# Performance work log

Measured on AMD Instinct MI355X. Metric: run time of the kernel, lower is better.

The kernel has to match this reference:

```python
import jax, jax.numpy as jnp
import numpy as np

H = 4        # num_heads
D = 16       # d_hid (per-head dim)
INF = 1e9


def setup_inputs() -> dict:
    key = jax.random.key(0)
    ks = jax.random.split(key, 8)
    T, R, DT, DZ = 4, 384, 64, 128
    t = jax.random.normal(ks[0], (T, R, R, DT), dtype=jnp.float32)
    z = jax.random.normal(ks[1], (R, R, DZ), dtype=jnp.float32)
    template_mask = jnp.ones((T,), dtype=jnp.float32)
    wq = jax.random.normal(ks[2], (DZ, H * D), dtype=jnp.float32) * 0.08
    wk = jax.random.normal(ks[3], (DT, H * D), dtype=jnp.float32) * 0.12
    wv = jax.random.normal(ks[4], (DT, H * D), dtype=jnp.float32) * 0.12
    wo = jax.random.normal(ks[5], (H * D, DZ), dtype=jnp.float32) * 0.12
    bo = jnp.zeros((DZ,), dtype=jnp.float32)
    return {"t": t, "z": z, "template_mask": template_mask,
            "wq": wq, "wk": wk, "wv": wv, "wo": wo, "bo": bo}


def reference(t, z, template_mask, wq, wk, wv, wo, bo):
    # t: [T, R, R, d_t], z: [R, R, d_z], template_mask: [T]
    R = z.shape[0]
    scale = 1.0 / np.sqrt(float(D))
    # gen_attn_mask: 0 where mask > 0, -inf where masked out
    bias = jnp.where(template_mask > 0.0, 0.0, -INF)          # [T]
    # permute_final_dims(t, (1,2,0,3)): template axis becomes kv length
    tp = jnp.transpose(t, (1, 2, 0, 3))                        # [R, R, T, d_t]
    # q_len is 1 (z.unsqueeze(-2)); fold it away
    q = (z @ wq).reshape(R, R, H, D) * scale                   # [R, R, H, D]
    k = (tp @ wk).reshape(R, R, -1, H, D)                      # [R, R, T, H, D]
    v = (tp @ wv).reshape(R, R, -1, H, D)                      # [R, R, T, H, D]
    logits = jnp.einsum('xyhd,xythd->xyht', q, k) + bias       # [R, R, H, T]
    a = jax.nn.softmax(logits, axis=-1)
    o = jnp.einsum('xyht,xythd->xyhd', a, v).reshape(R, R, H * D)
    return o @ wo + bo                                         # [R, R, d_z]
```

## Files before the change

### kernel.cpp

```cpp
#include <hip/hip_runtime.h>


typedef __bf16 bf16x8 __attribute__((ext_vector_type(8)));
typedef float f32x4 __attribute__((ext_vector_type(4)));
typedef unsigned int u32x4 __attribute__((ext_vector_type(4)));
typedef unsigned int u32x2 __attribute__((ext_vector_type(2)));

#define MFMA16(A, B, C) __builtin_amdgcn_mfma_f32_16x16x32_bf16((A), (B), (C), 0, 0, 0)

__device__ __forceinline__ unsigned int f2b_pk(float a, float b) {
  unsigned int ua = __float_as_uint(a), ub = __float_as_uint(b);
  ua = (ua + 0x7fffu + ((ua >> 16) & 1u)) >> 16;
  ub = (ub + 0x7fffu + ((ub >> 16) & 1u)) & 0xffff0000u;
  return ua | ub;
}

__device__ __forceinline__ bf16x8 ldg8(const float* p) {
  const float4* q = (const float4*)p;
  float4 a = q[0];
  float4 b = q[1];
  u32x4 u;
  u.x = f2b_pk(a.x, a.y);
  u.y = f2b_pk(a.z, a.w);
  u.z = f2b_pk(b.x, b.y);
  u.w = f2b_pk(b.z, b.w);
  return __builtin_bit_cast(bf16x8, u);
}

__device__ __forceinline__ bf16x8 ldsA(const char* smem, int baseByte, int row,
                                       int colElem, int strideElem) {
  int off = baseByte + (((row * strideElem + colElem) * 2) ^ ((row & 7) << 4));
  return __builtin_bit_cast(bf16x8, *(const u32x4*)(smem + off));
}

__global__ __launch_bounds__(256, 2)
void tpa_kernel(const float* __restrict__ t_, const float* __restrict__ z_,
                const float* __restrict__ mask_,
                const float* __restrict__ wq_, const float* __restrict__ wk_,
                const float* __restrict__ wv_, const float* __restrict__ wo_,
                const float* __restrict__ bo_, float* __restrict__ out_) {
  extern __shared__ char smem[];

  for (int i = threadIdx.x; i < 24576; i += 256) {
    float v;
    int off;
    if (i < 8192) {
      int r = i >> 7, cc = i & 127;
      v = wq_[cc * 64 + r] * 0.25f;
      off = 0 + ((i * 2) ^ ((r & 7) << 4));
    } else if (i < 12288) {
      int j = i - 8192, r = j >> 6, cc = j & 63;
      v = wk_[cc * 64 + r];
      off = 16384 + ((j * 2) ^ ((r & 7) << 4));
    } else if (i < 16384) {
      int j = i - 12288, r = j >> 6, cc = j & 63;
      v = wv_[cc * 64 + r];
      off = 24576 + ((j * 2) ^ ((r & 7) << 4));
    } else {
      int j = i - 16384, r = j >> 6, cc = j & 63;
      v = wo_[cc * 128 + r];
      off = 32768 + ((j * 2) ^ ((r & 7) << 4));
    }
    unsigned int u = __float_as_uint(v);
    *(unsigned short*)(smem + off) =
        (unsigned short)((u + 0x7fffu + ((u >> 16) & 1u)) >> 16);
  }
  __syncthreads();

  const int lane = threadIdx.x & 63;
  const int wid = threadIdx.x >> 6;
  const int c = lane & 15;
  const int g = lane >> 4;

  const float b0 = mask_[0] > 0.f ? 0.f : -1e9f;
  const float b1 = mask_[1] > 0.f ? 0.f : -1e9f;
  const float b2 = mask_[2] > 0.f ? 0.f : -1e9f;
  const float b3 = mask_[3] > 0.f ? 0.f : -1e9f;

  float4 bo_v[8];
#pragma unroll
  for (int m = 0; m < 8; ++m) bo_v[m] = *(const float4*)(bo_ + m * 16 + g * 4);

  char* Olds = smem + 49152 + wid * 2048;
  const f32x4 vz = {0.f, 0.f, 0.f, 0.f};

  for (int tile = blockIdx.x * 4 + wid; tile < 9216; tile += 2048) {
    const int p = tile * 16 + c;
    const float* zp = z_ + (size_t)p * 128;
    const float* tp = t_ + (size_t)p * 64;

    f32x4 qacc[4] = {vz, vz, vz, vz};
#pragma unroll
    for (int s = 0; s < 4; ++s) {
      bf16x8 zb = ldg8(zp + s * 32 + g * 8);
#pragma unroll
      for (int h = 0; h < 4; ++h)
        qacc[h] = MFMA16(ldsA(smem, 0, h * 16 + c, s * 32 + g * 8, 128), zb, qacc[h]);
    }

    f32x4 oacc[4] = {vz, vz, vz, vz};
    float ssum[4] = {0.f, 0.f, 0.f, 0.f};
#pragma unroll
    for (int tt = 0; tt < 4; ++tt) {
      const float* tq = tp + (size_t)tt * 9437184;
      bf16x8 tb0 = ldg8(tq + g * 8);
      bf16x8 tb1 = ldg8(tq + 32 + g * 8);
      f32x4 kacc[4] = {vz, vz, vz, vz};
      f32x4 vacc[4] = {vz, vz, vz, vz};
#pragma unroll
      for (int h = 0; h < 4; ++h) {
        kacc[h] = MFMA16(ldsA(smem, 16384, h * 16 + c, g * 8, 64), tb0, kacc[h]);
        kacc[h] = MFMA16(ldsA(smem, 16384, h * 16 + c, 32 + g * 8, 64), tb1, kacc[h]);
        vacc[h] = MFMA16(ldsA(smem, 24576, h * 16 + c, g * 8, 64), tb0, vacc[h]);
        vacc[h] = MFMA16(ldsA(smem, 24576, h * 16 + c, 32 + g * 8, 64), tb1, vacc[h]);
      }
      const float bt = (tt == 0) ? b0 : (tt == 1) ? b1 : (tt == 2) ? b2 : b3;
#pragma unroll
      for (int h = 0; h < 4; ++h) {
        float d = qacc[h][0] * kacc[h][0] + qacc[h][1] * kacc[h][1] +
                  qacc[h][2] * kacc[h][2] + qacc[h][3] * kacc[h][3];
        d += __shfl_xor(d, 16);
        d += __shfl_xor(d, 32);
        float e = __expf(d + bt);
        ssum[h] += e;
        oacc[h] += e * vacc[h];
      }
    }

#pragma unroll
    for (int h = 0; h < 4; ++h) {
      float inv = 1.0f / ssum[h];
      f32x4 o = oacc[h] * inv;
      u32x2 w;
      w.x = f2b_pk(o[0], o[1]);
      w.y = f2b_pk(o[2], o[3]);
      int off = (c * 128 + h * 32 + g * 8) ^ ((c & 7) << 4);
      *(u32x2*)(Olds + off) = w;
    }
    asm volatile("s_waitcnt lgkmcnt(0)" ::: "memory");

    f32x4 outacc[8] = {vz, vz, vz, vz, vz, vz, vz, vz};
#pragma unroll
    for (int s = 0; s < 2; ++s) {
      int off = (c * 128 + s * 64 + g * 16) ^ ((c & 7) << 4);
      bf16x8 ob = __builtin_bit_cast(bf16x8, *(const u32x4*)(Olds + off));
#pragma unroll
      for (int m = 0; m < 8; ++m)
        outacc[m] = MFMA16(ldsA(smem, 32768, m * 16 + c, s * 32 + g * 8, 64), ob, outacc[m]);
    }

    float* op = out_ + (size_t)p * 128;
#pragma unroll
    for (int m = 0; m < 8; ++m) {
      float4 bv = bo_v[m];
      float4 st;
      st.x = outacc[m][0] + bv.x;
      st.y = outacc[m][1] + bv.y;
      st.z = outacc[m][2] + bv.z;
      st.w = outacc[m][3] + bv.w;
      *(float4*)(op + m * 16 + g * 4) = st;
    }
    asm volatile("" ::: "memory");
  }
}

extern "C" void kernel_launch(void* const* d_in, const int* in_sizes, int n_in,
                              void* d_out, int out_size, void* d_ws, size_t ws_size,
                              hipStream_t stream) {
  const float* t = (const float*)d_in[0];
  const float* z = (const float*)d_in[1];
  const float* mk = (const float*)d_in[2];
  const float* wq = (const float*)d_in[3];
  const float* wk = (const float*)d_in[4];
  const float* wv = (const float*)d_in[5];
  const float* wo = (const float*)d_in[6];
  const float* bo = (const float*)d_in[7];
  float* out = (float*)d_out;
  (void)in_sizes; (void)n_in; (void)out_size; (void)d_ws; (void)ws_size;

  hipLaunchKernelGGL(tpa_kernel, dim3(512), dim3(256), 57344, stream,
                     t, z, mk, wq, wk, wv, wo, bo, out);
}
```

Baseline: 93.80 us.

## Double workgroup size, prefetch next template slice, and shrink register footprint

Raises the block to 512 threads (8 waves) with 64KB LDS and a launch bound of 4 blocks per SM, which doubles the waves resident per block. The t loads for the next template are software-prefetched while the current one is computed. K and V accumulators are now computed per head instead of all heads at once, and the bias is reloaded at store time rather than kept in registers. Together these aim to cut register pressure and raise memory-level parallelism, at the cost of more per-head MFMA dependency chains and larger LDS per block, which may limit blocks per CU.

```diff
diff --git a/kernel.cpp b/kernel.cpp
--- a/kernel.cpp
+++ b/kernel.cpp
@@ -15,10 +15,7 @@
   return ua | ub;
 }
 
-__device__ __forceinline__ bf16x8 ldg8(const float* p) {
-  const float4* q = (const float4*)p;
-  float4 a = q[0];
-  float4 b = q[1];
+__device__ __forceinline__ bf16x8 pack8(float4 a, float4 b) {
   u32x4 u;
   u.x = f2b_pk(a.x, a.y);
   u.y = f2b_pk(a.z, a.w);
@@ -27,13 +24,18 @@
   return __builtin_bit_cast(bf16x8, u);
 }
 
+__device__ __forceinline__ bf16x8 ldg8(const float* p) {
+  const float4* q = (const float4*)p;
+  return pack8(q[0], q[1]);
+}
+
 __device__ __forceinline__ bf16x8 ldsA(const char* smem, int baseByte, int row,
                                        int colElem, int strideElem) {
   int off = baseByte + (((row * strideElem + colElem) * 2) ^ ((row & 7) << 4));
   return __builtin_bit_cast(bf16x8, *(const u32x4*)(smem + off));
 }
 
-__global__ __launch_bounds__(256, 2)
+__global__ __launch_bounds__(512, 4)
 void tpa_kernel(const float* __restrict__ t_, const float* __restrict__ z_,
                 const float* __restrict__ mask_,
                 const float* __restrict__ wq_, const float* __restrict__ wk_,
@@ -41,7 +43,7 @@
                 const float* __restrict__ bo_, float* __restrict__ out_) {
   extern __shared__ char smem[];
 
-  for (int i = threadIdx.x; i < 24576; i += 256) {
+  for (int i = threadIdx.x; i < 24576; i += 512) {
     float v;
     int off;
     if (i < 8192) {
@@ -77,17 +79,18 @@
   const float b2 = mask_[2] > 0.f ? 0.f : -1e9f;
   const float b3 = mask_[3] > 0.f ? 0.f : -1e9f;
 
-  float4 bo_v[8];
-#pragma unroll
-  for (int m = 0; m < 8; ++m) bo_v[m] = *(const float4*)(bo_ + m * 16 + g * 4);
-
   char* Olds = smem + 49152 + wid * 2048;
   const f32x4 vz = {0.f, 0.f, 0.f, 0.f};
 
-  for (int tile = blockIdx.x * 4 + wid; tile < 9216; tile += 2048) {
+  for (int tile = blockIdx.x * 8 + wid; tile < 9216; tile += 4096) {
     const int p = tile * 16 + c;
     const float* zp = z_ + (size_t)p * 128;
     const float* tp = t_ + (size_t)p * 64;
+
+    float4 c0 = *(const float4*)(tp + g * 8);
+    float4 c1 = *(const float4*)(tp + g * 8 + 4);
+    float4 c2 = *(const float4*)(tp + 32 + g * 8);
+    float4 c3 = *(const float4*)(tp + 32 + g * 8 + 4);
 
     f32x4 qacc[4] = {vz, vz, vz, vz};
 #pragma unroll
@@ -102,29 +105,32 @@
     float ssum[4] = {0.f, 0.f, 0.f, 0.f};
 #pragma unroll
     for (int tt = 0; tt < 4; ++tt) {
-      const float* tq = tp + (size_t)tt * 9437184;
-      bf16x8 tb0 = ldg8(tq + g * 8);
-      bf16x8 tb1 = ldg8(tq + 32 + g * 8);
-      f32x4 kacc[4] = {vz, vz, vz, vz};
-      f32x4 vacc[4] = {vz, vz, vz, vz};
-#pragma unroll
-      for (int h = 0; h < 4; ++h) {
-        kacc[h] = MFMA16(ldsA(smem, 16384, h * 16 + c, g * 8, 64), tb0, kacc[h]);
-        kacc[h] = MFMA16(ldsA(smem, 16384, h * 16 + c, 32 + g * 8, 64), tb1, kacc[h]);
-        vacc[h] = MFMA16(ldsA(smem, 24576, h * 16 + c, g * 8, 64), tb0, vacc[h]);
-        vacc[h] = MFMA16(ldsA(smem, 24576, h * 16 + c, 32 + g * 8, 64), tb1, vacc[h]);
+      float4 n0, n1, n2, n3;
+      if (tt < 3) {
+        const float* tn = tp + (size_t)(tt + 1) * 9437184;
+        n0 = *(const float4*)(tn + g * 8);
+        n1 = *(const float4*)(tn + g * 8 + 4);
+        n2 = *(const float4*)(tn + 32 + g * 8);
+        n3 = *(const float4*)(tn + 32 + g * 8 + 4);
       }
+      bf16x8 tb0 = pack8(c0, c1);
+      bf16x8 tb1 = pack8(c2, c3);
       const float bt = (tt == 0) ? b0 : (tt == 1) ? b1 : (tt == 2) ? b2 : b3;
 #pragma unroll
       for (int h = 0; h < 4; ++h) {
-        float d = qacc[h][0] * kacc[h][0] + qacc[h][1] * kacc[h][1] +
-                  qacc[h][2] * kacc[h][2] + qacc[h][3] * kacc[h][3];
+        f32x4 kacc = MFMA16(ldsA(smem, 16384, h * 16 + c, g * 8, 64), tb0, vz);
+        kacc = MFMA16(ldsA(smem, 16384, h * 16 + c, 32 + g * 8, 64), tb1, kacc);
+        float d = qacc[h][0] * kacc[0] + qacc[h][1] * kacc[1] +
+                  qacc[h][2] * kacc[2] + qacc[h][3] * kacc[3];
         d += __shfl_xor(d, 16);
         d += __shfl_xor(d, 32);
         float e = __expf(d + bt);
         ssum[h] += e;
-        oacc[h] += e * vacc[h];
+        f32x4 vacc = MFMA16(ldsA(smem, 24576, h * 16 + c, g * 8, 64), tb0, vz);
+        vacc = MFMA16(ldsA(smem, 24576, h * 16 + c, 32 + g * 8, 64), tb1, vacc);
+        oacc[h] += e * vacc;
       }
+      if (tt < 3) { c0 = n0; c1 = n1; c2 = n2; c3 = n3; }
     }
 
 #pragma unroll
@@ -150,9 +156,10 @@
     }
 
     float* op = out_ + (size_t)p * 128;
+    const float4* bop = (const float4*)bo_;
 #pragma unroll
     for (int m = 0; m < 8; ++m) {
-      float4 bv = bo_v[m];
+      float4 bv = bop[m * 4 + g];
       float4 st;
       st.x = outacc[m][0] + bv.x;
       st.y = outacc[m][1] + bv.y;
@@ -178,6 +185,6 @@
   float* out = (float*)d_out;
   (void)in_sizes; (void)n_in; (void)out_size; (void)d_ws; (void)ws_size;
 
-  hipLaunchKernelGGL(tpa_kernel, dim3(512), dim3(256), 57344, stream,
+  hipLaunchKernelGGL(tpa_kernel, dim3(512), dim3(512), 65536, stream,
                      t, z, mk, wq, wk, wv, wo, bo, out);
 }
```

New measurement: 161.7 us. 72.4% more time.

## Split Q projection into separate kernel via workspace to raise occupancy

Applied to the files above, without the earlier changes.

Moves the z@wq projection into its own kernel that writes bf16 Q into the workspace. The main attention kernel then reads Q, needs less LDS and fewer registers, and runs with launch bounds of 4 blocks and 768 blocks instead of 2 and 512. The goal is higher occupancy and better latency hiding on the streaming t loads. The cost is an extra kernel launch plus a round trip of Q through global memory (about 19 MB written and read). The original fused kernel is kept as a fallback when the workspace is too small.

```diff
diff --git a/kernel.cpp b/kernel.cpp
--- a/kernel.cpp
+++ b/kernel.cpp
@@ -15,10 +15,7 @@
   return ua | ub;
 }
 
-__device__ __forceinline__ bf16x8 ldg8(const float* p) {
-  const float4* q = (const float4*)p;
-  float4 a = q[0];
-  float4 b = q[1];
+__device__ __forceinline__ bf16x8 pack8(float4 a, float4 b) {
   u32x4 u;
   u.x = f2b_pk(a.x, a.y);
   u.y = f2b_pk(a.z, a.w);
@@ -27,75 +24,102 @@
   return __builtin_bit_cast(bf16x8, u);
 }
 
+__device__ __forceinline__ bf16x8 ldg8(const float* p) {
+  const float4* q = (const float4*)p;
+  return pack8(q[0], q[1]);
+}
+
 __device__ __forceinline__ bf16x8 ldsA(const char* smem, int baseByte, int row,
                                        int colElem, int strideElem) {
   int off = baseByte + (((row * strideElem + colElem) * 2) ^ ((row & 7) << 4));
   return __builtin_bit_cast(bf16x8, *(const u32x4*)(smem + off));
 }
 
-__global__ __launch_bounds__(256, 2)
-void tpa_kernel(const float* __restrict__ t_, const float* __restrict__ z_,
-                const float* __restrict__ mask_,
-                const float* __restrict__ wq_, const float* __restrict__ wk_,
-                const float* __restrict__ wv_, const float* __restrict__ wo_,
-                const float* __restrict__ bo_, float* __restrict__ out_) {
+__device__ __forceinline__ void stage_w(char* smem, int off, float v, int r, int j) {
+  unsigned int u = __float_as_uint(v);
+  *(unsigned short*)(smem + off + ((j * 2) ^ ((r & 7) << 4))) =
+      (unsigned short)((u + 0x7fffu + ((u >> 16) & 1u)) >> 16);
+}
+
+__global__ __launch_bounds__(256, 4)
+void q_kernel(const float* __restrict__ z_, const float* __restrict__ wq_,
+              u32x2* __restrict__ q_) {
   extern __shared__ char smem[];
-
-  for (int i = threadIdx.x; i < 24576; i += 256) {
-    float v;
-    int off;
-    if (i < 8192) {
-      int r = i >> 7, cc = i & 127;
-      v = wq_[cc * 64 + r] * 0.25f;
-      off = 0 + ((i * 2) ^ ((r & 7) << 4));
-    } else if (i < 12288) {
-      int j = i - 8192, r = j >> 6, cc = j & 63;
-      v = wk_[cc * 64 + r];
-      off = 16384 + ((j * 2) ^ ((r & 7) << 4));
-    } else if (i < 16384) {
-      int j = i - 12288, r = j >> 6, cc = j & 63;
-      v = wv_[cc * 64 + r];
-      off = 24576 + ((j * 2) ^ ((r & 7) << 4));
-    } else {
-      int j = i - 16384, r = j >> 6, cc = j & 63;
-      v = wo_[cc * 128 + r];
-      off = 32768 + ((j * 2) ^ ((r & 7) << 4));
-    }
-    unsigned int u = __float_as_uint(v);
-    *(unsigned short*)(smem + off) =
-        (unsigned short)((u + 0x7fffu + ((u >> 16) & 1u)) >> 16);
+  for (int i = threadIdx.x; i < 8192; i += 256) {
+    int r = i >> 7, cc = i & 127;
+    stage_w(smem, 0, wq_[cc * 64 + r] * 0.25f, r, i);
   }
   __syncthreads();
-
   const int lane = threadIdx.x & 63;
   const int wid = threadIdx.x >> 6;
-  const int c = lane & 15;
-  const int g = lane >> 4;
+  const int c = lane & 15, g = lane >> 4;
+  const f32x4 vz = {0.f, 0.f, 0.f, 0.f};
+  for (int tile = blockIdx.x * 4 + wid; tile < 9216; tile += 3072) {
+    const int p = tile * 16 + c;
+    const float* zp = z_ + (size_t)p * 128;
+    f32x4 qacc[4] = {vz, vz, vz, vz};
+#pragma unroll
+    for (int s = 0; s < 4; ++s) {
+      bf16x8 zb = ldg8(zp + s * 32 + g * 8);
+#pragma unroll
+      for (int h = 0; h < 4; ++h)
+        qacc[h] = MFMA16(ldsA(smem, 0, h * 16 + c, s * 32 + g * 8, 128), zb, qacc[h]);
+    }
+#pragma unroll
+    for (int h = 0; h < 4; ++h) {
+      u32x2 w;
+      w.x = f2b_pk(qacc[h][0], qacc[h][1]);
+      w.y = f2b_pk(qacc[h][2], qacc[h][3]);
+      q_[(size_t)(tile * 4 + h) * 64 + lane] = w;
+    }
+  }
+}
+
+__global__ __launch_bounds__(256, 4)
+void tpa_b_kernel(const float* __restrict__ t_, const u32x2* __restrict__ q_,
+                  const float* __restrict__ mask_,
+                  const float* __restrict__ wk_, const float* __restrict__ wv_,
+                  const float* __restrict__ wo_, const float* __restrict__ bo_,
+                  float* __restrict__ out_) {
+  extern __shared__ char smem[];
+  for (int i = threadIdx.x; i < 16384; i += 256) {
+    if (i < 4096) {
+      int r = i >> 6, cc = i & 63;
+      stage_w(smem, 0, wk_[cc * 64 + r], r, i);
+    } else if (i < 8192) {
+      int j = i - 4096, r = j >> 6, cc = j & 63;
+      stage_w(smem, 8192, wv_[cc * 64 + r], r, j);
+    } else {
+      int j = i - 8192, r = j >> 6, cc = j & 63;
+      stage_w(smem, 16384, wo_[cc * 128 + r], r, j);
+    }
+  }
+  __syncthreads();
+
+  const int lane = threadIdx.x & 63;
+  const int wid = threadIdx.x >> 6;
+  const int c = lane & 15, g = lane >> 4;
 
   const float b0 = mask_[0] > 0.f ? 0.f : -1e9f;
   const float b1 = mask_[1] > 0.f ? 0.f : -1e9f;
   const float b2 = mask_[2] > 0.f ? 0.f : -1e9f;
   const float b3 = mask_[3] > 0.f ? 0.f : -1e9f;
 
-  float4 bo_v[8];
-#pragma unroll
-  for (int m = 0; m < 8; ++m) bo_v[m] = *(const float4*)(bo_ + m * 16 + g * 4);
-
-  char* Olds = smem + 49152 + wid * 2048;
+  char* Olds = smem + 32768 + wid * 2048;
   const f32x4 vz = {0.f, 0.f, 0.f, 0.f};
 
-  for (int tile = blockIdx.x * 4 + wid; tile < 9216; tile += 2048) {
+  for (int tile = blockIdx.x * 4 + wid; tile < 9216; tile += 3072) {
     const int p = tile * 16 + c;
-    const float* zp = z_ + (size_t)p * 128;
     const float* tp = t_ + (size_t)p * 64;
 
-    f32x4 qacc[4] = {vz, vz, vz, vz};
-#pragma unroll
-    for (int s = 0; s < 4; ++s) {
-      bf16x8 zb = ldg8(zp + s * 32 + g * 8);
-#pragma unroll
-      for (int h = 0; h < 4; ++h)
-        qacc[h] = MFMA16(ldsA(smem, 0, h * 16 + c, s * 32 + g * 8, 128), zb, qacc[h]);
+    f32x4 qacc[4];
+#pragma unroll
+    for (int h = 0; h < 4; ++h) {
+      u32x2 w = q_[(size_t)(tile * 4 + h) * 64 + lane];
+      qacc[h][0] = __uint_as_float(w.x << 16);
+      qacc[h][1] = __uint_as_float(w.x & 0xffff0000u);
+      qacc[h][2] = __uint_as_float(w.y << 16);
+      qacc[h][3] = __uint_as_float(w.y & 0xffff0000u);
     }
 
     f32x4 oacc[4] = {vz, vz, vz, vz};
@@ -105,14 +129,13 @@
       const float* tq = tp + (size_t)tt * 9437184;
       bf16x8 tb0 = ldg8(tq + g * 8);
       bf16x8 tb1 = ldg8(tq + 32 + g * 8);
-      f32x4 kacc[4] = {vz, vz, vz, vz};
-      f32x4 vacc[4] = {vz, vz, vz, vz};
+      f32x4 kacc[4], vacc[4];
 #pragma unroll
       for (int h = 0; h < 4; ++h) {
-        kacc[h] = MFMA16(ldsA(smem, 16384, h * 16 + c, g * 8, 64), tb0, kacc[h]);
-        kacc[h] = MFMA16(ldsA(smem, 16384, h * 16 + c, 32 + g * 8, 64), tb1, kacc[h]);
-        vacc[h] = MFMA16(ldsA(smem, 24576, h * 16 + c, g * 8, 64), tb0, vacc[h]);
-        vacc[h] = MFMA16(ldsA(smem, 24576, h * 16 + c, 32 + g * 8, 64), tb1, vacc[h]);
+        kacc[h] = MFMA16(ldsA(smem, 0, h * 16 + c, g * 8, 64), tb0, vz);
+        kacc[h] = MFMA16(ldsA(smem, 0, h * 16 + c, 32 + g * 8, 64), tb1, kacc[h]);
+        vacc[h] = MFMA16(ldsA(smem, 8192, h * 16 + c, g * 8, 64), tb0, vz);
+        vacc[h] = MFMA16(ldsA(smem, 8192, h * 16 + c, 32 + g * 8, 64), tb1, vacc[h]);
       }
       const float bt = (tt == 0) ? b0 : (tt == 1) ? b1 : (tt == 2) ? b2 : b3;
 #pragma unroll
@@ -146,13 +169,121 @@
       bf16x8 ob = __builtin_bit_cast(bf16x8, *(const u32x4*)(Olds + off));
 #pragma unroll
       for (int m = 0; m < 8; ++m)
+        outacc[m] = MFMA16(ldsA(smem, 16384, m * 16 + c, s * 32 + g * 8, 64), ob, outacc[m]);
+    }
+
+    float* op = out_ + (size_t)p * 128;
+    const float4* bop = (const float4*)bo_;
+#pragma unroll
+    for (int m = 0; m < 8; ++m) {
+      float4 bv = bop[m * 4 + g];
+      float4 st;
+      st.x = outacc[m][0] + bv.x;
+      st.y = outacc[m][1] + bv.y;
+      st.z = outacc[m][2] + bv.z;
+      st.w = outacc[m][3] + bv.w;
+      *(float4*)(op + m * 16 + g * 4) = st;
+    }
+    asm volatile("" ::: "memory");
+  }
+}
+
+__global__ __launch_bounds__(256, 2)
+void tpa_fused(const float* __restrict__ t_, const float* __restrict__ z_,
+               const float* __restrict__ mask_,
+               const float* __restrict__ wq_, const float* __restrict__ wk_,
+               const float* __restrict__ wv_, const float* __restrict__ wo_,
+               const float* __restrict__ bo_, float* __restrict__ out_) {
+  extern __shared__ char smem[];
+  for (int i = threadIdx.x; i < 24576; i += 256) {
+    if (i < 8192) {
+      int r = i >> 7;
+      stage_w(smem, 0, wq_[(i & 127) * 64 + r] * 0.25f, r, i);
+    } else if (i < 12288) {
+      int j = i - 8192, r = j >> 6;
+      stage_w(smem, 16384, wk_[(j & 63) * 64 + r], r, j);
+    } else if (i < 16384) {
+      int j = i - 12288, r = j >> 6;
+      stage_w(smem, 24576, wv_[(j & 63) * 64 + r], r, j);
+    } else {
+      int j = i - 16384, r = j >> 6;
+      stage_w(smem, 32768, wo_[(j & 63) * 128 + r], r, j);
+    }
+  }
+  __syncthreads();
+  const int lane = threadIdx.x & 63;
+  const int wid = threadIdx.x >> 6;
+  const int c = lane & 15, g = lane >> 4;
+  const float b0 = mask_[0] > 0.f ? 0.f : -1e9f;
+  const float b1 = mask_[1] > 0.f ? 0.f : -1e9f;
+  const float b2 = mask_[2] > 0.f ? 0.f : -1e9f;
+  const float b3 = mask_[3] > 0.f ? 0.f : -1e9f;
+  char* Olds = smem + 49152 + wid * 2048;
+  const f32x4 vz = {0.f, 0.f, 0.f, 0.f};
+  for (int tile = blockIdx.x * 4 + wid; tile < 9216; tile += 2048) {
+    const int p = tile * 16 + c;
+    const float* zp = z_ + (size_t)p * 128;
+    const float* tp = t_ + (size_t)p * 64;
+    f32x4 qacc[4] = {vz, vz, vz, vz};
+#pragma unroll
+    for (int s = 0; s < 4; ++s) {
+      bf16x8 zb = ldg8(zp + s * 32 + g * 8);
+#pragma unroll
+      for (int h = 0; h < 4; ++h)
+        qacc[h] = MFMA16(ldsA(smem, 0, h * 16 + c, s * 32 + g * 8, 128), zb, qacc[h]);
+    }
+    f32x4 oacc[4] = {vz, vz, vz, vz};
+    float ssum[4] = {0.f, 0.f, 0.f, 0.f};
+#pragma unroll
+    for (int tt = 0; tt < 4; ++tt) {
+      const float* tq = tp + (size_t)tt * 9437184;
+      bf16x8 tb0 = ldg8(tq + g * 8);
+      bf16x8 tb1 = ldg8(tq + 32 + g * 8);
+      f32x4 kacc[4], vacc[4];
+#pragma unroll
+      for (int h = 0; h < 4; ++h) {
+        kacc[h] = MFMA16(ldsA(smem, 16384, h * 16 + c, g * 8, 64), tb0, vz);
+        kacc[h] = MFMA16(ldsA(smem, 16384, h * 16 + c, 32 + g * 8, 64), tb1, kacc[h]);
+        vacc[h] = MFMA16(ldsA(smem, 24576, h * 16 + c, g * 8, 64), tb0, vz);
+        vacc[h] = MFMA16(ldsA(smem, 24576, h * 16 + c, 32 + g * 8, 64), tb1, vacc[h]);
+      }
+      const float bt = (tt == 0) ? b0 : (tt == 1) ? b1 : (tt == 2) ? b2 : b3;
+#pragma unroll
+      for (int h = 0; h < 4; ++h) {
+        float d = qacc[h][0] * kacc[h][0] + qacc[h][1] * kacc[h][1] +
+                  qacc[h][2] * kacc[h][2] + qacc[h][3] * kacc[h][3];
+        d += __shfl_xor(d, 16);
+        d += __shfl_xor(d, 32);
+        float e = __expf(d + bt);
+        ssum[h] += e;
+        oacc[h] += e * vacc[h];
+      }
+    }
+#pragma unroll
+    for (int h = 0; h < 4; ++h) {
+      float inv = 1.0f / ssum[h];
+      f32x4 o = oacc[h] * inv;
+      u32x2 w;
+      w.x = f2b_pk(o[0], o[1]);
+      w.y = f2b_pk(o[2], o[3]);
+      int off = (c * 128 + h * 32 + g * 8) ^ ((c & 7) << 4);
+      *(u32x2*)(Olds + off) = w;
+    }
+    asm volatile("s_waitcnt lgkmcnt(0)" ::: "memory");
+    f32x4 outacc[8] = {vz, vz, vz, vz, vz, vz, vz, vz};
+#pragma unroll
+    for (int s = 0; s < 2; ++s) {
+      int off = (c * 128 + s * 64 + g * 16) ^ ((c & 7) << 4);
+      bf16x8 ob = __builtin_bit_cast(bf16x8, *(const u32x4*)(Olds + off));
+#pragma unroll
+      for (int m = 0; m < 8; ++m)
         outacc[m] = MFMA16(ldsA(smem, 32768, m * 16 + c, s * 32 + g * 8, 64), ob, outacc[m]);
     }
-
     float* op = out_ + (size_t)p * 128;
+    const float4* bop = (const float4*)bo_;
 #pragma unroll
     for (int m = 0; m < 8; ++m) {
-      float4 bv = bo_v[m];
+      float4 bv = bop[m * 4 + g];
       float4 st;
       st.x = outacc[m][0] + bv.x;
       st.y = outacc[m][1] + bv.y;
@@ -176,8 +307,16 @@
   const float* wo = (const float*)d_in[6];
   const float* bo = (const float*)d_in[7];
   float* out = (float*)d_out;
-  (void)in_sizes; (void)n_in; (void)out_size; (void)d_ws; (void)ws_size;
-
-  hipLaunchKernelGGL(tpa_kernel, dim3(512), dim3(256), 57344, stream,
-                     t, z, mk, wq, wk, wv, wo, bo, out);
-}
+  (void)in_sizes; (void)n_in; (void)out_size;
+
+  const size_t qbytes = (size_t)9216 * 4 * 64 * 8;
+  if (ws_size >= qbytes) {
+    u32x2* qws = (u32x2*)d_ws;
+    hipLaunchKernelGGL(q_kernel, dim3(768), dim3(256), 16384, stream, z, wq, qws);
+    hipLaunchKernelGGL(tpa_b_kernel, dim3(768), dim3(256), 40960, stream,
+                       t, qws, mk, wk, wv, wo, bo, out);
+  } else {
+    hipLaunchKernelGGL(tpa_fused, dim3(512), dim3(256), 57344, stream,
+                       t, z, mk, wq, wk, wv, wo, bo, out);
+  }
+}
```

Measured after the change: 174.2 us. +85.7%, slower.
